# Kernel optimization log

Hardware: AMD Instinct MI355X
Metric: run time of the kernel (lower is better)

## Reference

```python
import jax, jax.numpy as jnp
import numpy as np

N = 100000       # nodes
NFEAT = 1024     # input feature dim
HIDDEN = 64      # args.hidden
NCLASS = 16
K = 2            # args.k -> r_final width = (2**(K+1)-1)*HIDDEN = 448
E1 = 1_600_000   # 1-hop edges (avg deg 16)
E2 = 8_000_000   # strict 2-hop edges (avg deg 80)


def _sym_norm_vals(rows, cols, n):
    # D^{-1/2} A D^{-1/2} values for binary adjacency (matches _adj_norm)
    deg = jnp.zeros((n,), jnp.float32).at[rows].add(1.0)
    d = jnp.where(deg > 0, deg ** -0.5, 0.0)
    return d[rows] * d[cols]


def setup_inputs() -> dict:
    key = jax.random.key(0)
    k1, k2, k3, k4, k5 = jax.random.split(key, 5)
    x = jax.random.normal(k1, (N, NFEAT), jnp.float32)
    a1_idx = jax.random.randint(k2, (2, E1), 0, N, dtype=jnp.int32)
    a2_idx = jax.random.randint(k3, (2, E2), 0, N, dtype=jnp.int32)
    a1_val = _sym_norm_vals(a1_idx[0], a1_idx[1], N)
    a2_val = _sym_norm_vals(a2_idx[0], a2_idx[1], N)
    # xavier_uniform init, matching reset_parameter()
    lim_e = (6.0 / (NFEAT + HIDDEN)) ** 0.5
    w_embed = jax.random.uniform(k4, (NFEAT, HIDDEN), jnp.float32, -lim_e, lim_e)
    out_in = (2 ** (K + 1) - 1) * HIDDEN
    lim_c = (6.0 / (out_in + NCLASS)) ** 0.5
    w_classify = jax.random.uniform(k5, (out_in, NCLASS), jnp.float32, -lim_c, lim_c)
    return {"x": x, "a1_idx": a1_idx, "a1_val": a1_val,
            "a2_idx": a2_idx, "a2_val": a2_val,
            "w_embed": w_embed, "w_classify": w_classify}


def _spmm(idx, val, dense, n):
    # sparse [n,n] (COO rows=idx[0], cols=idx[1]) @ dense [n,d]
    return jax.ops.segment_sum(val[:, None] * dense[idx[1]], idx[0], num_segments=n)


def reference(x, a1_idx, a1_val, a2_idx, a2_val, w_embed, w_classify):
    n = x.shape[0]
    rs = [jax.nn.relu(x @ w_embed)]                      # [n, h]
    for _ in range(K):
        r = rs[-1]
        r1 = _spmm(a1_idx, a1_val, r, n)
        r2 = _spmm(a2_idx, a2_val, r, n)
        rs.append(jnp.concatenate([r1, r2], axis=1))     # width doubles each step
    r_final = jnp.concatenate(rs, axis=1)                # [n, 7h]; dropout is identity in eval
    return jax.nn.log_softmax(r_final @ w_classify, axis=1)
```

## Files before the change

kernel.cpp:

```cpp
#include <hip/hip_runtime.h>

constexpr int NFEAT = 1024;
constexpr int HID   = 64;
constexpr int NC    = 16;

typedef __attribute__((ext_vector_type(8))) short bf16x8;
typedef __attribute__((ext_vector_type(4))) float f32x4;

__device__ inline unsigned short f2bf(float f) {
  unsigned u = __float_as_uint(f);
  unsigned r = u + 0x7FFFu + ((u >> 16) & 1u);
  return (unsigned short)(r >> 16);
}

__global__ __launch_bounds__(256) void k_bhist(const int* __restrict__ rows, int* __restrict__ bcount,
                                               int e, int nb) {
  __shared__ int hist[512];
  int t = threadIdx.x;
  for (int i = t; i < nb; i += 256) hist[i] = 0;
  __syncthreads();
  int e0 = blockIdx.x * 4096;
#pragma unroll
  for (int j = 0; j < 16; ++j) {
    int idx = e0 + j * 256 + t;
    if (idx < e) atomicAdd(&hist[rows[idx] >> 8], 1);
  }
  __syncthreads();
  for (int i = t; i < nb; i += 256) {
    int c = hist[i];
    if (c) atomicAdd(&bcount[i], c);
  }
}

__global__ __launch_bounds__(512) void k_bscan(const int* __restrict__ c1, const int* __restrict__ c2,
                                               int* __restrict__ s1, int* __restrict__ s2,
                                               int* __restrict__ bc1, int* __restrict__ bc2, int nb) {
  __shared__ int sh[512];
  int t = threadIdx.x;
  for (int g = 0; g < 2; ++g) {
    const int* c = g ? c2 : c1;
    int* s  = g ? s2 : s1;
    int* bc = g ? bc2 : bc1;
    int v = (t < nb) ? c[t] : 0;
    sh[t] = v;
    __syncthreads();
    for (int off = 1; off < 512; off <<= 1) {
      int x = (t >= off) ? sh[t - off] : 0;
      __syncthreads();
      sh[t] += x;
      __syncthreads();
    }
    int excl = (t > 0) ? sh[t - 1] : 0;
    if (t < nb) { s[t] = excl; bc[t] = excl; }
    if (t == nb - 1) s[nb] = sh[t];
    __syncthreads();
  }
}

__global__ __launch_bounds__(256) void k_bin(const int* __restrict__ rows, const int* __restrict__ cols,
                                             int* __restrict__ bcur, unsigned* __restrict__ stg,
                                             int e, int nb) {
  __shared__ int hist[512];
  __shared__ int cur[512];
  int t = threadIdx.x;
  for (int i = t; i < nb; i += 256) hist[i] = 0;
  __syncthreads();
  int e0 = blockIdx.x * 4096;
  int rr[16], cc[16];
#pragma unroll
  for (int j = 0; j < 16; ++j) {
    int idx = e0 + j * 256 + t;
    if (idx < e) {
      rr[j] = rows[idx];
      cc[j] = cols[idx];
      atomicAdd(&hist[rr[j] >> 8], 1);
    } else rr[j] = -1;
  }
  __syncthreads();
  for (int i = t; i < nb; i += 256) {
    int c = hist[i];
    cur[i] = c ? atomicAdd(&bcur[i], c) : 0;
  }
  __syncthreads();
#pragma unroll
  for (int j = 0; j < 16; ++j) {
    if (rr[j] >= 0) {
      int b = rr[j] >> 8;
      int p = atomicAdd(&cur[b], 1);
      stg[p] = ((unsigned)(rr[j] & 255) << 17) | (unsigned)cc[j];
    }
  }
}

__global__ __launch_bounds__(256) void k_debin(const unsigned* __restrict__ stg, const int* __restrict__ bstart,
                                               int* __restrict__ rp, int* __restrict__ pos,
                                               float* __restrict__ d, int* __restrict__ csr, int n) {
  __shared__ int hist[256];
  __shared__ int offs[256];
  __shared__ int cur[256];
  int b = blockIdx.x, t = threadIdx.x;
  int start = bstart[b], next = bstart[b + 1];
  hist[t] = 0;
  __syncthreads();
  for (int i = start + t; i < next; i += 256)
    atomicAdd(&hist[stg[i] >> 17], 1);
  __syncthreads();
  int v = hist[t];
  offs[t] = v;
  __syncthreads();
  for (int off = 1; off < 256; off <<= 1) {
    int x = (t >= off) ? offs[t - off] : 0;
    __syncthreads();
    offs[t] += x;
    __syncthreads();
  }
  int excl = start + ((t > 0) ? offs[t - 1] : 0);
  cur[t] = excl;
  int row_g = (b << 8) + t;
  if (row_g < n) {
    rp[row_g]  = excl;
    pos[row_g] = excl + v;
    d[row_g]   = (v > 0) ? 1.0f / sqrtf((float)v) : 0.0f;
  }
  __syncthreads();
  for (int i = start + t; i < next; i += 256) {
    unsigned pk = stg[i];
    int ro = (int)(pk >> 17);
    int col = (int)(pk & 0x1FFFFu);
    int p = atomicAdd(&cur[ro], 1);
    csr[p] = col;
  }
}

__global__ __launch_bounds__(256) void k_embed(const float* __restrict__ x, const float* __restrict__ we,
                                               const float* __restrict__ wcl,
                                               const float* __restrict__ d1, const float* __restrict__ d2,
                                               float* __restrict__ T, int n) {
  __shared__ float pool[7168];
  __shared__ float rs[64 * 68];
  unsigned short* xs  = (unsigned short*)pool;
  unsigned short* wsb = (unsigned short*)(pool + 2304);

  const int t    = threadIdx.x;
  const int w    = t >> 6;
  const int l    = t & 63;
  const int quad = l >> 4;
  const int lr   = l & 15;
  const int br   = blockIdx.x * 64;

  const int sxr = t >> 2;
  const int sxc = (t & 3) * 4;
  const int xrow = min(br + sxr, n - 1);
  const float* xp = x + (size_t)xrow * NFEAT;
  const int swn = t & 63;
  const int swk = (t >> 6) * 4;

  f32x4 acc[4];
#pragma unroll
  for (int i = 0; i < 4; ++i) acc[i] = (f32x4){0.f, 0.f, 0.f, 0.f};

  for (int kc = 0; kc < NFEAT; kc += 64) {
    float4 xv[4];
#pragma unroll
    for (int j = 0; j < 4; ++j) xv[j] = *(const float4*)(xp + kc + j * 16 + sxc);
    float wv[16];
#pragma unroll
    for (int p = 0; p < 4; ++p)
#pragma unroll
      for (int i = 0; i < 4; ++i)
        wv[p * 4 + i] = we[(size_t)(kc + p * 16 + swk + i) * HID + swn];
    __syncthreads();
#pragma unroll
    for (int j = 0; j < 4; ++j) {
      ushort4 u;
      u.x = f2bf(xv[j].x); u.y = f2bf(xv[j].y); u.z = f2bf(xv[j].z); u.w = f2bf(xv[j].w);
      *(ushort4*)&xs[sxr * 72 + j * 16 + sxc] = u;
    }
#pragma unroll
    for (int p = 0; p < 4; ++p) {
      ushort4 u;
      u.x = f2bf(wv[p * 4 + 0]); u.y = f2bf(wv[p * 4 + 1]);
      u.z = f2bf(wv[p * 4 + 2]); u.w = f2bf(wv[p * 4 + 3]);
      *(ushort4*)&wsb[swn * 72 + p * 16 + swk] = u;
    }
    __syncthreads();
#pragma unroll
    for (int ks = 0; ks < 2; ++ks) {
      bf16x8 af = *(const bf16x8*)&xs[(w * 16 + lr) * 72 + ks * 32 + quad * 8];
#pragma unroll
      for (int nt = 0; nt < 4; ++nt) {
        bf16x8 bfr = *(const bf16x8*)&wsb[(nt * 16 + lr) * 72 + ks * 32 + quad * 8];
        acc[nt] = __builtin_amdgcn_mfma_f32_16x16x32_bf16(af, bfr, acc[nt], 0, 0, 0);
      }
    }
  }
  __syncthreads();

#pragma unroll
  for (int nt = 0; nt < 4; ++nt)
#pragma unroll
    for (int r = 0; r < 4; ++r)
      rs[(w * 16 + quad * 4 + r) * 68 + nt * 16 + lr] = fmaxf(acc[nt][r], 0.f);

  const int srcblk[7] = {0, 1, 2, 3, 5, 4, 6};
  for (int i = t; i < 7168; i += 256) {
    int k = i / 112, c = i % 112;
    int p = c >> 4, cc = c & 15;
    pool[i] = wcl[(size_t)(64 * srcblk[p] + k) * NC + cc];
  }
  __syncthreads();

  const int prow = t >> 2, pcg = t & 3;
  float4 ap[7];
#pragma unroll
  for (int j = 0; j < 7; ++j) ap[j] = make_float4(0.f, 0.f, 0.f, 0.f);
  for (int k = 0; k < 64; ++k) {
    float rv = rs[prow * 68 + k];
#pragma unroll
    for (int j = 0; j < 7; ++j) {
      float4 w4 = *(const float4*)&pool[k * 112 + pcg * 28 + j * 4];
      ap[j].x += rv * w4.x; ap[j].y += rv * w4.y; ap[j].z += rv * w4.z; ap[j].w += rv * w4.w;
    }
  }
  int gr = br + prow;
  if (gr < n) {
    size_t sn = (size_t)n;
    float d1v = d1[gr], d2v = d2[gr];
#pragma unroll
    for (int j = 0; j < 7; ++j) {
      int c = pcg * 28 + j * 4;
      int p = c >> 4, cc = c & 15;
      float s = (p < 3) ? 1.0f : ((p < 5) ? d1v : d2v);
      float4 v = ap[j];
      v.x *= s; v.y *= s; v.z *= s; v.w *= s;
      size_t o;
      if (p < 3)      o = (size_t)p * 16 * sn + (size_t)gr * 16 + cc;
      else if (p < 5) o = 48 * sn + (size_t)gr * 32 + ((p == 4) ? 16 : 0) + cc;
      else            o = 80 * sn + (size_t)gr * 32 + ((p == 6) ? 16 : 0) + cc;
      *(float4*)(T + o) = v;
    }
  }
}

template <int L>
__global__ __launch_bounds__(256) void k_spmm(const int* __restrict__ rp, const int* __restrict__ re,
                                              const int* __restrict__ cols, const float* __restrict__ d,
                                              const float* __restrict__ src, float* __restrict__ dst, int n) {
  int t = blockIdx.x * 256 + threadIdx.x;
  int row = t / L;
  if (row >= n) return;
  int sub = t % L;
  int e = rp[row], end = re[row];
  const float4* s4 = (const float4*)src;
  float4 acc = make_float4(0.f, 0.f, 0.f, 0.f);
  for (; e < end; ++e) {
    int c = cols[e];
    float4 g = s4[(size_t)c * L + sub];
    acc.x += g.x; acc.y += g.y; acc.z += g.z; acc.w += g.w;
  }
  float s = d[row];
  acc.x *= s; acc.y *= s; acc.z *= s; acc.w *= s;
  ((float4*)dst)[(size_t)row * L + sub] = acc;
}

__global__ __launch_bounds__(256) void k_combine(float* __restrict__ t1, float* __restrict__ t2,
                                                 const float* __restrict__ P1, const float* __restrict__ P2,
                                                 const float* __restrict__ d1, const float* __restrict__ d2,
                                                 int n) {
  int t = blockIdx.x * 256 + threadIdx.x;
  if (t >= n * 4) return;
  int row = t >> 2, c = t & 3;
  float s1 = d1[row], s2 = d2[row];
  float4* T1 = (float4*)t1;
  float4* T2 = (float4*)t2;
  const float4* p1 = (const float4*)P1;
  const float4* p2 = (const float4*)P2;
  float4 a = T1[t], u = p1[(size_t)row * 8 + c], w = p2[(size_t)row * 8 + c];
  a.x = (a.x + u.x + w.x) * s1; a.y = (a.y + u.y + w.y) * s1;
  a.z = (a.z + u.z + w.z) * s1; a.w = (a.w + u.w + w.w) * s1;
  T1[t] = a;
  float4 b = T2[t];
  u = p1[(size_t)row * 8 + 4 + c]; w = p2[(size_t)row * 8 + 4 + c];
  b.x = (b.x + u.x + w.x) * s2; b.y = (b.y + u.y + w.y) * s2;
  b.z = (b.z + u.z + w.z) * s2; b.w = (b.w + u.w + w.w) * s2;
  T2[t] = b;
}

__global__ __launch_bounds__(256) void k_final(const float* __restrict__ t0, const float* __restrict__ zA,
                                               const float* __restrict__ zB, float* __restrict__ out, int n) {
  int row = blockIdx.x * 256 + threadIdx.x;
  if (row >= n) return;
  const float4* a4 = (const float4*)t0;
  const float4* b4 = (const float4*)zA;
  const float4* c4 = (const float4*)zB;
  float z[16];
#pragma unroll
  for (int j = 0; j < 4; ++j) {
    float4 a = a4[(size_t)row * 4 + j], b = b4[(size_t)row * 4 + j], c = c4[(size_t)row * 4 + j];
    z[j * 4 + 0] = a.x + b.x + c.x;
    z[j * 4 + 1] = a.y + b.y + c.y;
    z[j * 4 + 2] = a.z + b.z + c.z;
    z[j * 4 + 3] = a.w + b.w + c.w;
  }
  float m = z[0];
#pragma unroll
  for (int i = 1; i < 16; ++i) m = fmaxf(m, z[i]);
  float s = 0.f;
#pragma unroll
  for (int i = 0; i < 16; ++i) s += expf(z[i] - m);
  float lg = m + logf(s);
  float4* o4 = (float4*)out;
#pragma unroll
  for (int j = 0; j < 4; ++j) {
    float4 o;
    o.x = z[j * 4 + 0] - lg; o.y = z[j * 4 + 1] - lg;
    o.z = z[j * 4 + 2] - lg; o.w = z[j * 4 + 3] - lg;
    o4[(size_t)row * 4 + j] = o;
  }
}

extern "C" void kernel_launch(void* const* d_in, const int* in_sizes, int n_in,
                              void* d_out, int out_size, void* d_ws, size_t ws_size,
                              hipStream_t stream) {
  const float* x   = (const float*)d_in[0];
  const int*   a1i = (const int*)d_in[1];
  const int*   a2i = (const int*)d_in[3];
  const float* we  = (const float*)d_in[5];
  const float* wcl = (const float*)d_in[6];
  float* out = (float*)d_out;

  const int n  = in_sizes[0] / NFEAT;
  const int e1 = in_sizes[2];
  const int e2 = in_sizes[4];
  const int nb = (n + 255) / 256;

  char* ws = (char*)d_ws;
  size_t off = 0;
  auto alloc = [&](size_t bytes) -> void* {
    void* p = ws + off;
    off += (bytes + 255) & ~(size_t)255;
    return p;
  };
  float* t0 = (float*)alloc((size_t)n * 16 * 4);
  float* t1 = (float*)alloc((size_t)n * 16 * 4);
  float* t2 = (float*)alloc((size_t)n * 16 * 4);
  float* U1 = (float*)alloc((size_t)n * 32 * 4);
  float* U2 = (float*)alloc((size_t)n * 32 * 4);
  float* P1 = (float*)alloc((size_t)n * 32 * 4);
  float* P2 = (float*)alloc((size_t)n * 32 * 4);
  int* rp1  = (int*)alloc((size_t)n * 4);
  int* pos1 = (int*)alloc((size_t)n * 4);
  int* rp2  = (int*)alloc((size_t)n * 4);
  int* pos2 = (int*)alloc((size_t)n * 4);
  float* d1 = (float*)alloc((size_t)n * 4);
  float* d2 = (float*)alloc((size_t)n * 4);
  int*      col1 = (int*)alloc((size_t)e1 * 4);
  int*      col2 = (int*)alloc((size_t)e2 * 4);
  unsigned* stg1 = (unsigned*)alloc((size_t)e1 * 4);
  unsigned* stg2 = (unsigned*)alloc((size_t)e2 * 4);
  int* bcnt1 = (int*)alloc(4096);
  int* bcnt2 = (int*)alloc(4096);
  int* bst1  = (int*)alloc(4096);
  int* bst2  = (int*)alloc(4096);
  int* bc1   = (int*)alloc(4096);
  int* bc2   = (int*)alloc(4096);
  float* zA = U1;
  float* zB = U2;

  (void)ws_size; (void)n_in; (void)out_size;

  hipMemsetAsync(bcnt1, 0, (size_t)nb * 4, stream);
  hipMemsetAsync(bcnt2, 0, (size_t)nb * 4, stream);

  k_bhist<<<(e1 + 4095) / 4096, 256, 0, stream>>>(a1i, bcnt1, e1, nb);
  k_bhist<<<(e2 + 4095) / 4096, 256, 0, stream>>>(a2i, bcnt2, e2, nb);

  k_bscan<<<1, 512, 0, stream>>>(bcnt1, bcnt2, bst1, bst2, bc1, bc2, nb);

  k_bin<<<(e1 + 4095) / 4096, 256, 0, stream>>>(a1i, a1i + e1, bc1, stg1, e1, nb);
  k_bin<<<(e2 + 4095) / 4096, 256, 0, stream>>>(a2i, a2i + e2, bc2, stg2, e2, nb);

  k_debin<<<nb, 256, 0, stream>>>(stg1, bst1, rp1, pos1, d1, col1, n);
  k_debin<<<nb, 256, 0, stream>>>(stg2, bst2, rp2, pos2, d2, col2, n);

  k_embed<<<(n + 63) / 64, 256, 0, stream>>>(x, we, wcl, d1, d2, t0, n);

  k_spmm<8><<<(n * 8 + 255) / 256, 256, 0, stream>>>(rp1, pos1, col1, d1, U1, P1, n);
  k_spmm<8><<<(n * 8 + 255) / 256, 256, 0, stream>>>(rp2, pos2, col2, d2, U2, P2, n);

  k_combine<<<(n * 4 + 255) / 256, 256, 0, stream>>>(t1, t2, P1, P2, d1, d2, n);

  k_spmm<4><<<(n * 4 + 255) / 256, 256, 0, stream>>>(rp1, pos1, col1, d1, t1, zA, n);
  k_spmm<4><<<(n * 4 + 255) / 256, 256, 0, stream>>>(rp2, pos2, col2, d2, t2, zB, n);

  k_final<<<(n + 255) / 256, 256, 0, stream>>>(t0, zA, zB, out, n);
}
```

Baseline: 1.302 ms.

## Fuse SpMM stages into two kernels and store gathered features as bf16

Replaces the two pairs of per-adjacency SpMM launches plus the combine and final kernels with two fused kernels. Each fused kernel walks both adjacencies per row and applies the combine or log-softmax in its epilogue, using shuffles for the row reduction. Gather sources U1/U2 and the intermediates p/q are now stored in bf16, which halves the bytes moved by the random gathers. The cost is bf16 rounding error in the propagated features and less parallelism per row in the fused loops.

```diff
diff --git a/kernel.cpp b/kernel.cpp
--- a/kernel.cpp
+++ b/kernel.cpp
@@ -6,12 +6,15 @@
 
 typedef __attribute__((ext_vector_type(8))) short bf16x8;
 typedef __attribute__((ext_vector_type(4))) float f32x4;
+typedef __attribute__((ext_vector_type(8))) unsigned short u16x8;
 
 __device__ inline unsigned short f2bf(float f) {
   unsigned u = __float_as_uint(f);
   unsigned r = u + 0x7FFFu + ((u >> 16) & 1u);
   return (unsigned short)(r >> 16);
 }
+__device__ inline float bflo(unsigned u) { return __uint_as_float(u << 16); }
+__device__ inline float bfhi(unsigned u) { return __uint_as_float(u & 0xFFFF0000u); }
 
 __global__ __launch_bounds__(256) void k_bhist(const int* __restrict__ rows, int* __restrict__ bcount,
                                                int e, int nb) {
@@ -135,7 +138,9 @@
 __global__ __launch_bounds__(256) void k_embed(const float* __restrict__ x, const float* __restrict__ we,
                                                const float* __restrict__ wcl,
                                                const float* __restrict__ d1, const float* __restrict__ d2,
-                                               float* __restrict__ T, int n) {
+                                               float* __restrict__ T,
+                                               unsigned short* __restrict__ U1, unsigned short* __restrict__ U2,
+                                               int n) {
   __shared__ float pool[7168];
   __shared__ float rs[64 * 68];
   unsigned short* xs  = (unsigned short*)pool;
@@ -229,94 +234,117 @@
 #pragma unroll
     for (int j = 0; j < 7; ++j) {
       int c = pcg * 28 + j * 4;
-      int p = c >> 4, cc = c & 15;
-      float s = (p < 3) ? 1.0f : ((p < 5) ? d1v : d2v);
+      int pb = c >> 4, cc = c & 15;
       float4 v = ap[j];
-      v.x *= s; v.y *= s; v.z *= s; v.w *= s;
-      size_t o;
-      if (p < 3)      o = (size_t)p * 16 * sn + (size_t)gr * 16 + cc;
-      else if (p < 5) o = 48 * sn + (size_t)gr * 32 + ((p == 4) ? 16 : 0) + cc;
-      else            o = 80 * sn + (size_t)gr * 32 + ((p == 6) ? 16 : 0) + cc;
-      *(float4*)(T + o) = v;
-    }
-  }
-}
-
-template <int L>
-__global__ __launch_bounds__(256) void k_spmm(const int* __restrict__ rp, const int* __restrict__ re,
-                                              const int* __restrict__ cols, const float* __restrict__ d,
-                                              const float* __restrict__ src, float* __restrict__ dst, int n) {
+      if (pb < 3) {
+        size_t o = (size_t)pb * 16 * sn + (size_t)gr * 16 + cc;
+        *(float4*)(T + o) = v;
+      } else {
+        float s = (pb < 5) ? d1v : d2v;
+        v.x *= s; v.y *= s; v.z *= s; v.w *= s;
+        ushort4 u;
+        u.x = f2bf(v.x); u.y = f2bf(v.y); u.z = f2bf(v.z); u.w = f2bf(v.w);
+        unsigned short* Ub = (pb < 5) ? U1 : U2;
+        int half = (pb == 4 || pb == 6) ? 16 : 0;
+        *(ushort4*)(Ub + (size_t)gr * 32 + half + cc) = u;
+      }
+    }
+  }
+}
+
+__global__ __launch_bounds__(256) void k_inner(const int* __restrict__ rp1, const int* __restrict__ pe1,
+                                               const int* __restrict__ col1,
+                                               const int* __restrict__ rp2, const int* __restrict__ pe2,
+                                               const int* __restrict__ col2,
+                                               const float* __restrict__ d1, const float* __restrict__ d2,
+                                               const unsigned short* __restrict__ U1,
+                                               const unsigned short* __restrict__ U2,
+                                               const float* __restrict__ t1, const float* __restrict__ t2,
+                                               unsigned short* __restrict__ p, unsigned short* __restrict__ q,
+                                               int n) {
   int t = blockIdx.x * 256 + threadIdx.x;
-  int row = t / L;
+  int row = t >> 2;
   if (row >= n) return;
-  int sub = t % L;
-  int e = rp[row], end = re[row];
-  const float4* s4 = (const float4*)src;
-  float4 acc = make_float4(0.f, 0.f, 0.f, 0.f);
-  for (; e < end; ++e) {
-    int c = cols[e];
-    float4 g = s4[(size_t)c * L + sub];
-    acc.x += g.x; acc.y += g.y; acc.z += g.z; acc.w += g.w;
-  }
-  float s = d[row];
-  acc.x *= s; acc.y *= s; acc.z *= s; acc.w *= s;
-  ((float4*)dst)[(size_t)row * L + sub] = acc;
-}
-
-__global__ __launch_bounds__(256) void k_combine(float* __restrict__ t1, float* __restrict__ t2,
-                                                 const float* __restrict__ P1, const float* __restrict__ P2,
-                                                 const float* __restrict__ d1, const float* __restrict__ d2,
-                                                 int n) {
+  int sub = t & 3;
+  float a1[8] = {0, 0, 0, 0, 0, 0, 0, 0};
+  float a2[8] = {0, 0, 0, 0, 0, 0, 0, 0};
+  for (int e = rp1[row], end = pe1[row]; e < end; ++e) {
+    int c = col1[e];
+    uint4 v = *(const uint4*)(U1 + (size_t)c * 32 + sub * 8);
+    a1[0] += bflo(v.x); a1[1] += bfhi(v.x);
+    a1[2] += bflo(v.y); a1[3] += bfhi(v.y);
+    a1[4] += bflo(v.z); a1[5] += bfhi(v.z);
+    a1[6] += bflo(v.w); a1[7] += bfhi(v.w);
+  }
+  for (int e = rp2[row], end = pe2[row]; e < end; ++e) {
+    int c = col2[e];
+    uint4 v = *(const uint4*)(U2 + (size_t)c * 32 + sub * 8);
+    a2[0] += bflo(v.x); a2[1] += bfhi(v.x);
+    a2[2] += bflo(v.y); a2[3] += bfhi(v.y);
+    a2[4] += bflo(v.z); a2[5] += bfhi(v.z);
+    a2[6] += bflo(v.w); a2[7] += bfhi(v.w);
+  }
+  float s1 = d1[row], s2 = d2[row];
+  const float* tb = (sub < 2) ? (t1 + (size_t)row * 16 + sub * 8)
+                              : (t2 + (size_t)row * 16 + (sub - 2) * 8);
+  unsigned short* dst = (sub < 2) ? (p + (size_t)row * 16 + sub * 8)
+                                  : (q + (size_t)row * 16 + (sub - 2) * 8);
+  float so = (sub < 2) ? s1 : s2;
+  float4 b0 = *(const float4*)tb;
+  float4 b1 = *(const float4*)(tb + 4);
+  float bb[8] = {b0.x, b0.y, b0.z, b0.w, b1.x, b1.y, b1.z, b1.w};
+  u16x8 us;
+#pragma unroll
+  for (int i = 0; i < 8; ++i) {
+    float v = so * (bb[i] + s1 * a1[i] + s2 * a2[i]);
+    us[i] = f2bf(v);
+  }
+  *(u16x8*)dst = us;
+}
+
+__global__ __launch_bounds__(256) void k_outer(const int* __restrict__ rp1, const int* __restrict__ pe1,
+                                               const int* __restrict__ col1,
+                                               const int* __restrict__ rp2, const int* __restrict__ pe2,
+                                               const int* __restrict__ col2,
+                                               const float* __restrict__ d1, const float* __restrict__ d2,
+                                               const unsigned short* __restrict__ p,
+                                               const unsigned short* __restrict__ q,
+                                               const float* __restrict__ t0, float* __restrict__ out,
+                                               int n) {
   int t = blockIdx.x * 256 + threadIdx.x;
-  if (t >= n * 4) return;
-  int row = t >> 2, c = t & 3;
+  int row = t >> 2;
+  if (row >= n) return;
+  int sub = t & 3;
+  float a[4] = {0, 0, 0, 0}, b[4] = {0, 0, 0, 0};
+  for (int e = rp1[row], end = pe1[row]; e < end; ++e) {
+    int c = col1[e];
+    uint2 v = *(const uint2*)(p + (size_t)c * 16 + sub * 4);
+    a[0] += bflo(v.x); a[1] += bfhi(v.x);
+    a[2] += bflo(v.y); a[3] += bfhi(v.y);
+  }
+  for (int e = rp2[row], end = pe2[row]; e < end; ++e) {
+    int c = col2[e];
+    uint2 v = *(const uint2*)(q + (size_t)c * 16 + sub * 4);
+    b[0] += bflo(v.x); b[1] += bfhi(v.x);
+    b[2] += bflo(v.y); b[3] += bfhi(v.y);
+  }
   float s1 = d1[row], s2 = d2[row];
-  float4* T1 = (float4*)t1;
-  float4* T2 = (float4*)t2;
-  const float4* p1 = (const float4*)P1;
-  const float4* p2 = (const float4*)P2;
-  float4 a = T1[t], u = p1[(size_t)row * 8 + c], w = p2[(size_t)row * 8 + c];
-  a.x = (a.x + u.x + w.x) * s1; a.y = (a.y + u.y + w.y) * s1;
-  a.z = (a.z + u.z + w.z) * s1; a.w = (a.w + u.w + w.w) * s1;
-  T1[t] = a;
-  float4 b = T2[t];
-  u = p1[(size_t)row * 8 + 4 + c]; w = p2[(size_t)row * 8 + 4 + c];
-  b.x = (b.x + u.x + w.x) * s2; b.y = (b.y + u.y + w.y) * s2;
-  b.z = (b.z + u.z + w.z) * s2; b.w = (b.w + u.w + w.w) * s2;
-  T2[t] = b;
-}
-
-__global__ __launch_bounds__(256) void k_final(const float* __restrict__ t0, const float* __restrict__ zA,
-                                               const float* __restrict__ zB, float* __restrict__ out, int n) {
-  int row = blockIdx.x * 256 + threadIdx.x;
-  if (row >= n) return;
-  const float4* a4 = (const float4*)t0;
-  const float4* b4 = (const float4*)zA;
-  const float4* c4 = (const float4*)zB;
-  float z[16];
-#pragma unroll
-  for (int j = 0; j < 4; ++j) {
-    float4 a = a4[(size_t)row * 4 + j], b = b4[(size_t)row * 4 + j], c = c4[(size_t)row * 4 + j];
-    z[j * 4 + 0] = a.x + b.x + c.x;
-    z[j * 4 + 1] = a.y + b.y + c.y;
-    z[j * 4 + 2] = a.z + b.z + c.z;
-    z[j * 4 + 3] = a.w + b.w + c.w;
-  }
-  float m = z[0];
-#pragma unroll
-  for (int i = 1; i < 16; ++i) m = fmaxf(m, z[i]);
-  float s = 0.f;
-#pragma unroll
-  for (int i = 0; i < 16; ++i) s += expf(z[i] - m);
+  float4 t0v = *(const float4*)(t0 + (size_t)row * 16 + sub * 4);
+  float z[4];
+  z[0] = t0v.x + s1 * a[0] + s2 * b[0];
+  z[1] = t0v.y + s1 * a[1] + s2 * b[1];
+  z[2] = t0v.z + s1 * a[2] + s2 * b[2];
+  z[3] = t0v.w + s1 * a[3] + s2 * b[3];
+  float m = fmaxf(fmaxf(z[0], z[1]), fmaxf(z[2], z[3]));
+  m = fmaxf(m, __shfl_xor(m, 1));
+  m = fmaxf(m, __shfl_xor(m, 2));
+  float s = expf(z[0] - m) + expf(z[1] - m) + expf(z[2] - m) + expf(z[3] - m);
+  s += __shfl_xor(s, 1);
+  s += __shfl_xor(s, 2);
   float lg = m + logf(s);
-  float4* o4 = (float4*)out;
-#pragma unroll
-  for (int j = 0; j < 4; ++j) {
-    float4 o;
-    o.x = z[j * 4 + 0] - lg; o.y = z[j * 4 + 1] - lg;
-    o.z = z[j * 4 + 2] - lg; o.w = z[j * 4 + 3] - lg;
-    o4[(size_t)row * 4 + j] = o;
-  }
+  float4 o;
+  o.x = z[0] - lg; o.y = z[1] - lg; o.z = z[2] - lg; o.w = z[3] - lg;
+  *(float4*)(out + (size_t)row * 16 + sub * 4) = o;
 }
 
 extern "C" void kernel_launch(void* const* d_in, const int* in_sizes, int n_in,
@@ -344,10 +372,10 @@
   float* t0 = (float*)alloc((size_t)n * 16 * 4);
   float* t1 = (float*)alloc((size_t)n * 16 * 4);
   float* t2 = (float*)alloc((size_t)n * 16 * 4);
-  float* U1 = (float*)alloc((size_t)n * 32 * 4);
-  float* U2 = (float*)alloc((size_t)n * 32 * 4);
-  float* P1 = (float*)alloc((size_t)n * 32 * 4);
-  float* P2 = (float*)alloc((size_t)n * 32 * 4);
+  unsigned short* U1 = (unsigned short*)alloc((size_t)n * 32 * 2);
+  unsigned short* U2 = (unsigned short*)alloc((size_t)n * 32 * 2);
+  unsigned short* pp = (unsigned short*)alloc((size_t)n * 16 * 2);
+  unsigned short* qq = (unsigned short*)alloc((size_t)n * 16 * 2);
   int* rp1  = (int*)alloc((size_t)n * 4);
   int* pos1 = (int*)alloc((size_t)n * 4);
   int* rp2  = (int*)alloc((size_t)n * 4);
@@ -364,8 +392,6 @@
   int* bst2  = (int*)alloc(4096);
   int* bc1   = (int*)alloc(4096);
   int* bc2   = (int*)alloc(4096);
-  float* zA = U1;
-  float* zB = U2;
 
   (void)ws_size; (void)n_in; (void)out_size;
 
@@ -383,15 +409,11 @@
   k_debin<<<nb, 256, 0, stream>>>(stg1, bst1, rp1, pos1, d1, col1, n);
   k_debin<<<nb, 256, 0, stream>>>(stg2, bst2, rp2, pos2, d2, col2, n);
 
-  k_embed<<<(n + 63) / 64, 256, 0, stream>>>(x, we, wcl, d1, d2, t0, n);
-
-  k_spmm<8><<<(n * 8 + 255) / 256, 256, 0, stream>>>(rp1, pos1, col1, d1, U1, P1, n);
-  k_spmm<8><<<(n * 8 + 255) / 256, 256, 0, stream>>>(rp2, pos2, col2, d2, U2, P2, n);
-
-  k_combine<<<(n * 4 + 255) / 256, 256, 0, stream>>>(t1, t2, P1, P2, d1, d2, n);
-
-  k_spmm<4><<<(n * 4 + 255) / 256, 256, 0, stream>>>(rp1, pos1, col1, d1, t1, zA, n);
-  k_spmm<4><<<(n * 4 + 255) / 256, 256, 0, stream>>>(rp2, pos2, col2, d2, t2, zB, n);
-
-  k_final<<<(n + 255) / 256, 256, 0, stream>>>(t0, zA, zB, out, n);
-}
+  k_embed<<<(n + 63) / 64, 256, 0, stream>>>(x, we, wcl, d1, d2, t0, U1, U2, n);
+
+  k_inner<<<(n * 4 + 255) / 256, 256, 0, stream>>>(rp1, pos1, col1, rp2, pos2, col2,
+                                                   d1, d2, U1, U2, t1, t2, pp, qq, n);
+
+  k_outer<<<(n * 4 + 255) / 256, 256, 0, stream>>>(rp1, pos1, col1, rp2, pos2, col2,
+                                                   d1, d2, pp, qq, t0, out, n);
+}
```

Measured after the change: 1.187 ms. 1.1x faster.
